# Kernel optimization log

Measured on AMD Instinct MI355X. Metric: run time of the kernel, lower is better.

The kernel has to match this reference:

```python
import jax, jax.numpy as jnp
import numpy as np

EPS_NORM = 1e-12
BN_EPS = 1e-5
TEMP = 0.07


def _l2norm(x, axis):
    n = jnp.sqrt(jnp.sum(x * x, axis=axis, keepdims=True))
    return x / jnp.maximum(n, EPS_NORM)


def _bn_eval(z, w, b):
    # inference-mode BatchNorm2d with running_mean=0, running_var=1
    s = w / jnp.sqrt(jnp.asarray(1.0 + BN_EPS, z.dtype))
    return z * s[None, :, None, None] + b[None, :, None, None]


def setup_inputs() -> dict:
    key = jax.random.key(0)
    ks = jax.random.split(key, 8)
    B, C, H, W = 16, 256, 64, 64
    KD, P = 128, 256
    x = jax.random.normal(ks[0], (B, C, H, W), jnp.float32)
    m_features = jax.random.normal(ks[1], (P, KD), jnp.float32)
    q_w = jax.random.normal(ks[2], (KD, C), jnp.float32) * 0.05
    k_w = jax.random.normal(ks[3], (KD, KD), jnp.float32) * 0.05
    v_w = jax.random.normal(ks[4], (KD, KD), jnp.float32) * 0.05
    o_w = jax.random.normal(ks[5], (C, KD), jnp.float32) * 0.05
    dw_w = jax.random.normal(ks[6], (C, 1, 3, 3), jnp.float32) * 0.1
    return {
        "x": x, "m_features": m_features,
        "q_w": q_w, "q_b": jnp.zeros((KD,), jnp.float32),
        "k_w": k_w, "k_b": jnp.zeros((KD,), jnp.float32),
        "v_w": v_w, "v_b": jnp.zeros((KD,), jnp.float32),
        "o_w": o_w, "o_b": jnp.zeros((C,), jnp.float32),
        "dw_w": dw_w,
        "bn1_w": jnp.ones((C,), jnp.float32), "bn1_b": jnp.zeros((C,), jnp.float32),
        "bn2_w": jnp.ones((C,), jnp.float32), "bn2_b": jnp.zeros((C,), jnp.float32),
        "gamma": jnp.ones((C,), jnp.float32) * 1e-5,
    }


def reference(x, m_features, q_w, q_b, k_w, k_b, v_w, v_b, o_w, o_b,
              dw_w, bn1_w, bn1_b, bn2_w, bn2_b, gamma):
    B, C, H, W = x.shape
    KD = q_w.shape[0]
    residual = x
    # q_proj 1x1 conv -> [B,KD,H,W], L2-normalize over channel dim
    q = jnp.einsum('bchw,kc->bkhw', x, q_w) + q_b[None, :, None, None]
    q = _l2norm(q, axis=1)
    q = q.reshape(B, KD, H * W).transpose(0, 2, 1)  # [B, HW, KD]
    # k/v projections of memory bank [P, KD]
    k = _l2norm(m_features @ k_w.T + k_b, axis=-1)
    v = m_features @ v_w.T + v_b
    # fp32 attention with clamped logits
    q32, k32, v32 = q.astype(jnp.float32), k.astype(jnp.float32), v.astype(jnp.float32)
    logits = jnp.clip(jnp.einsum('bnd,pd->bnp', q32, k32) / TEMP, -30.0, 30.0)
    attn = jax.nn.softmax(logits, axis=-1)
    out = jnp.einsum('bnp,pd->bnd', attn, v32).astype(x.dtype)
    out = out.transpose(0, 2, 1).reshape(B, KD, H, W)
    # out_proj 1x1 conv -> [B,C,H,W]
    out = jnp.einsum('bkhw,ck->bchw', out, o_w) + o_b[None, :, None, None]
    # local branch: depthwise 3x3 conv + BN + exact GELU
    local = jax.lax.conv_general_dilated(
        out, dw_w, window_strides=(1, 1), padding='SAME',
        feature_group_count=C,
        dimension_numbers=('NCHW', 'OIHW', 'NCHW'))
    local = jax.nn.gelu(_bn_eval(local, bn1_w, bn1_b), approximate=False)
    out = out + local
    return _bn_eval(residual + out * gamma[None, :, None, None], bn2_w, bn2_b)
```

## Files before the change

### kernel.cpp

```cpp
#include <hip/hip_runtime.h>
#include <hip/hip_bf16.h>
#include <math.h>

#define B_ 16
#define C_ 256
#define H_ 64
#define W_ 64
#define KD_ 128
#define P_ 256
#define HW_ (H_ * W_)

typedef __bf16 bf16;
typedef float f32x4_t __attribute__((ext_vector_type(4)));
typedef float f32x16_t __attribute__((ext_vector_type(16)));
typedef unsigned char u8;

__device__ __forceinline__ unsigned cvt_pk_fp8_lo(float a, float b, unsigned old) {
#if __has_builtin(__builtin_amdgcn_cvt_pk_fp8_f32)
    return __builtin_amdgcn_cvt_pk_fp8_f32(a, b, old, false);
#else
    unsigned r = old;
    asm("v_cvt_pk_fp8_f32 %0, %1, %2" : "+v"(r) : "v"(a), "v"(b));
    return r;
#endif
}
__device__ __forceinline__ unsigned cvt_pk_fp8_hi(float a, float b, unsigned old) {
#if __has_builtin(__builtin_amdgcn_cvt_pk_fp8_f32)
    return __builtin_amdgcn_cvt_pk_fp8_f32(a, b, old, true);
#else
    unsigned r = old;
    asm("v_cvt_pk_fp8_f32 %0, %1, %2 op_sel:[0,0,1]" : "+v"(r) : "v"(a), "v"(b));
    return r;
#endif
}
__device__ __forceinline__ uint2 pack8_fp8(const float* f) {
    uint2 r;
    r.x = cvt_pk_fp8_hi(f[2], f[3], cvt_pk_fp8_lo(f[0], f[1], 0u));
    r.y = cvt_pk_fp8_hi(f[6], f[7], cvt_pk_fp8_lo(f[4], f[5], 0u));
    return r;
}
template<int SEL>
__device__ __forceinline__ float fp8_to_f32(unsigned w) {
#if __has_builtin(__builtin_amdgcn_cvt_f32_fp8)
    return __builtin_amdgcn_cvt_f32_fp8(w, SEL);
#else
    float r;
    asm("v_cvt_f32_fp8 %0, %1" : "=v"(r) : "v"(w >> (SEL * 8)));
    return r;
#endif
}

__global__ __launch_bounds__(128) void k_prep1(
    const float* __restrict__ m_feat,
    const float* __restrict__ k_w, const float* __restrict__ k_b,
    const float* __restrict__ v_w, const float* __restrict__ v_b,
    float* __restrict__ kn_f, float* __restrict__ v_f)
{
    const int p = blockIdx.x;
    const int j = threadIdx.x;
    __shared__ float msh[KD_];
    __shared__ float red[2];
    msh[j] = m_feat[p * KD_ + j];
    __syncthreads();

    float ka = k_b[j];
    float va = v_b[j];
#pragma unroll 4
    for (int d = 0; d < KD_; ++d) {
        const float m = msh[d];
        ka = fmaf(m, k_w[j * KD_ + d], ka);
        va = fmaf(m, v_w[j * KD_ + d], va);
    }
    float s = ka * ka;
#pragma unroll
    for (int o = 1; o < 64; o <<= 1) s += __shfl_xor(s, o);
    if ((j & 63) == 0) red[j >> 6] = s;
    __syncthreads();
    s = red[0] + red[1];
    const float inv = 1.0f / (0.07f * fmaxf(sqrtf(s), 1e-12f));
    kn_f[p * KD_ + j] = ka * inv;
    v_f[p * KD_ + j] = va;
}

__global__ __launch_bounds__(256) void k_prep23(
    const float* __restrict__ o_w, const float* __restrict__ v_f,
    const float* __restrict__ q_w, const float* __restrict__ kn_f,
    u8* __restrict__ m28, u8* __restrict__ qw8, u8* __restrict__ kn8)
{
    if (blockIdx.x < 256) {
        const int c = blockIdx.x;
        const int p = threadIdx.x;
        __shared__ float osh[KD_];
        if (p < KD_) osh[p] = o_w[c * KD_ + p];
        __syncthreads();
        float acc = 0.f;
#pragma unroll 4
        for (int k = 0; k < KD_; ++k) acc = fmaf(osh[k], v_f[p * KD_ + k], acc);
        const int mt = c >> 5, r = c & 31;
        const int ks = p >> 4, sub = (p >> 3) & 1, jj = p & 7;
        const unsigned pk = cvt_pk_fp8_lo(acc * 16.0f, 0.f, 0u);
        m28[(((mt * 16 + ks) * 64) + sub * 32 + r) * 8 + jj] = (u8)(pk & 0xffu);
    } else {
        const int t = (blockIdx.x - 256) * 256 + threadIdx.x;
        float f[8];
        if (t < 4096) {
            const int lane = t & 63, g = t >> 6, mt = g >> 4, ks = g & 15;
            const int row = mt * 32 + (lane & 31), k0 = ks * 16 + (lane >> 5) * 8;
            const float* src = q_w + row * C_ + k0;
#pragma unroll
            for (int j = 0; j < 8; ++j) f[j] = src[j] * 16.0f;
            ((uint2*)qw8)[t] = pack8_fp8(f);
        } else {
            const int u = t - 4096;
            const int lane = u & 63, g = u >> 6, mt = g >> 3, ks = g & 7;
            const int row = mt * 32 + (lane & 31), k0 = ks * 16 + (lane >> 5) * 8;
            const float* src = kn_f + row * KD_ + k0;
#pragma unroll
            for (int j = 0; j < 8; ++j) f[j] = src[j];
            ((uint2*)kn8)[u] = pack8_fp8(f);
        }
    }
}

__global__ __launch_bounds__(512, 4) void k_attn(
    const float* __restrict__ x,
    const float* __restrict__ q_b, const float* __restrict__ o_b,
    const u8* __restrict__ qw8, const u8* __restrict__ kn8,
    const u8* __restrict__ m28, u8* __restrict__ outf8)
{
    __shared__ __align__(16) char lds[75776];
    char* const xs = lds + 32768;
    float* const ss_lds   = (float*)(lds + 65536);
    float* const pmax_lds = (float*)(lds + 67584);
    float* const sum_lds  = (float*)(lds + 71680);

    const int rp = blockIdx.x;
    const int b = blockIdx.y;
    const int tid = threadIdx.x;
    const int lane = tid & 63;
    const int wid = tid >> 6;
    const int l31 = lane & 31;
    const int kh  = lane >> 5;

    long kna[8];
#pragma unroll
    for (int ks = 0; ks < 8; ++ks)
        kna[ks] = *(const long*)(kn8 + ((wid * 8 + ks) * 64 + lane) * 8);

    {
        const int sub = tid & 31;
        const int ch0 = tid >> 5;
        const float* xb = x + (size_t)b * C_ * HW_ + rp * 128 + sub * 4;
#pragma unroll
        for (int it = 0; it < 16; ++it) {
            const int ch = it * 16 + ch0;
            const f32x4_t v = *(const f32x4_t*)(xb + (size_t)ch * HW_);
            const unsigned w = cvt_pk_fp8_hi(v[2], v[3],
                               cvt_pk_fp8_lo(v[0], v[1], 0u));
            *(unsigned*)(lds + ch * 128 + sub * 4) = w;
        }
    }
    __syncthreads();

    {
        const int p  = tid & 127;
        const int cb = tid >> 7;
#pragma unroll
        for (int g = 0; g < 8; ++g) {
            const int c0 = cb * 64 + g * 8;
            union { u8 by[8]; uint2 u; } pk;
#pragma unroll
            for (int j = 0; j < 8; ++j)
                pk.by[j] = *(const u8*)(lds + (c0 + j) * 128 + p);
            *(uint2*)(xs + p * 256 + (c0 ^ ((p & 31) << 3))) = pk.u;
        }
    }
    __syncthreads();

    const int mtA = wid & 3, nh = wid >> 2;
    {
        f32x16_t qacc0, qacc1;
#pragma unroll
        for (int i = 0; i < 16; ++i) { qacc0[i] = 0.f; qacc1[i] = 0.f; }
#pragma unroll
        for (int ks = 0; ks < 16; ++ks) {
            const long a = *(const long*)(qw8 + ((mtA * 16 + ks) * 64 + lane) * 8);
            const int ko = (ks * 16 + kh * 8) ^ (l31 << 3);
            const long bx0 = *(const long*)(xs + (nh * 64 + l31) * 256 + ko);
            const long bx1 = *(const long*)(xs + (nh * 64 + 32 + l31) * 256 + ko);
            qacc0 = __builtin_amdgcn_mfma_f32_32x32x16_fp8_fp8(a, bx0, qacc0, 0, 0, 0);
            qacc1 = __builtin_amdgcn_mfma_f32_32x32x16_fp8_fp8(a, bx1, qacc1, 0, 0, 0);
        }
#pragma unroll
        for (int nt = 0; nt < 2; ++nt) {
            const int pix = nh * 64 + nt * 32 + l31;
            float ssp = 0.f;
#pragma unroll
            for (int g = 0; g < 4; ++g) {
                const f32x4_t qbv = *(const f32x4_t*)(q_b + mtA * 32 + g * 8 + kh * 4);
#pragma unroll
                for (int i = 0; i < 4; ++i) {
                    float qv = (nt == 0) ? qacc0[g * 4 + i] : qacc1[g * 4 + i];
                    qv += 16.0f * qbv[i];
                    if (nt == 0) qacc0[g * 4 + i] = qv; else qacc1[g * 4 + i] = qv;
                    ssp = fmaf(qv, qv, ssp);
                }
            }
            ssp += __shfl_xor(ssp, 32);
            if (lane < 32) ss_lds[pix * 4 + mtA] = ssp;
#pragma unroll
            for (int g = 0; g < 4; ++g) {
                const float e0 = (nt == 0) ? qacc0[g * 4 + 0] : qacc1[g * 4 + 0];
                const float e1 = (nt == 0) ? qacc0[g * 4 + 1] : qacc1[g * 4 + 1];
                const float e2 = (nt == 0) ? qacc0[g * 4 + 2] : qacc1[g * 4 + 2];
                const float e3 = (nt == 0) ? qacc0[g * 4 + 3] : qacc1[g * 4 + 3];
                const unsigned qw_ = cvt_pk_fp8_hi(e2, e3, cvt_pk_fp8_lo(e0, e1, 0u));
                *(unsigned*)(lds + pix * 128 +
                             ((mtA * 32 + g * 8 + kh * 4) ^ ((l31 & 15) << 3))) = qw_;
            }
        }
    }
    __syncthreads();

    f32x16_t lacc0, lacc1, lacc2, lacc3;
#pragma unroll
    for (int i = 0; i < 16; ++i) { lacc0[i] = 0.f; lacc1[i] = 0.f; lacc2[i] = 0.f; lacc3[i] = 0.f; }
#pragma unroll
    for (int ks = 0; ks < 8; ++ks) {
        const int ko = (ks * 16 + kh * 8) ^ ((l31 & 15) << 3);
        const long bq0 = *(const long*)(lds + (0 * 32 + l31) * 128 + ko);
        const long bq1 = *(const long*)(lds + (1 * 32 + l31) * 128 + ko);
        const long bq2 = *(const long*)(lds + (2 * 32 + l31) * 128 + ko);
        const long bq3 = *(const long*)(lds + (3 * 32 + l31) * 128 + ko);
        lacc0 = __builtin_amdgcn_mfma_f32_32x32x16_fp8_fp8(kna[ks], bq0, lacc0, 0, 0, 0);
        lacc1 = __builtin_amdgcn_mfma_f32_32x32x16_fp8_fp8(kna[ks], bq1, lacc1, 0, 0, 0);
        lacc2 = __builtin_amdgcn_mfma_f32_32x32x16_fp8_fp8(kna[ks], bq2, lacc2, 0, 0, 0);
        lacc3 = __builtin_amdgcn_mfma_f32_32x32x16_fp8_fp8(kna[ks], bq3, lacc3, 0, 0, 0);
    }
#pragma unroll
    for (int nt = 0; nt < 4; ++nt) {
        const int pix = nt * 32 + l31;
        float mx = -1e30f;
#pragma unroll
        for (int i = 0; i < 16; ++i) {
            const float lv = (nt == 0) ? lacc0[i] : (nt == 1) ? lacc1[i]
                           : (nt == 2) ? lacc2[i] : lacc3[i];
            mx = fmaxf(mx, lv);
        }
        mx = fmaxf(mx, __shfl_xor(mx, 32));
        if (lane < 32) pmax_lds[pix * 8 + wid] = mx;
    }
    __syncthreads();

#pragma unroll
    for (int nt = 0; nt < 4; ++nt) {
        const int pix = nt * 32 + l31;
        const f32x4_t s4 = *(const f32x4_t*)(ss_lds + pix * 4);
        const float qinv = 1.0f / fmaxf(sqrtf(s4[0] + s4[1] + s4[2] + s4[3]), 1e-12f);
        const f32x4_t ma = *(const f32x4_t*)(pmax_lds + pix * 8);
        const f32x4_t mb = *(const f32x4_t*)(pmax_lds + pix * 8 + 4);
        const float cof = 5.545177444479562f -
                          fmaxf(fmaxf(fmaxf(ma[0], ma[1]), fmaxf(ma[2], ma[3])),
                                fmaxf(fmaxf(mb[0], mb[1]), fmaxf(mb[2], mb[3]))) * qinv;
        float sm = 0.f;
#pragma unroll
        for (int g = 0; g < 4; ++g) {
            float e[4];
#pragma unroll
            for (int i = 0; i < 4; ++i) {
                const float lv = (nt == 0) ? lacc0[g * 4 + i] : (nt == 1) ? lacc1[g * 4 + i]
                               : (nt == 2) ? lacc2[g * 4 + i] : lacc3[g * 4 + i];
                e[i] = __expf(fmaf(lv, qinv, cof));
                sm += e[i];
            }
            const unsigned ew = cvt_pk_fp8_hi(e[2], e[3],
                                cvt_pk_fp8_lo(e[0], e[1], 0u));
            const int p0 = wid * 32 + g * 8 + kh * 4;
            *(unsigned*)(lds + pix * 256 + (p0 ^ (l31 << 3))) = ew;
        }
        sm += __shfl_xor(sm, 32);
        if (lane < 32) sum_lds[pix * 8 + wid] = sm;
    }
    __syncthreads();

    f32x16_t oacc0, oacc1, oacc2, oacc3;
#pragma unroll
    for (int i = 0; i < 16; ++i) { oacc0[i] = 0.f; oacc1[i] = 0.f; oacc2[i] = 0.f; oacc3[i] = 0.f; }
#pragma unroll
    for (int ks = 0; ks < 16; ++ks) {
        const long a = *(const long*)(m28 + ((wid * 16 + ks) * 64 + lane) * 8);
        const int ko = (ks * 16 + kh * 8);
        const long be0 = *(const long*)(lds + (0 * 32 + l31) * 256 + (ko ^ (l31 << 3)));
        const long be1 = *(const long*)(lds + (1 * 32 + l31) * 256 + (ko ^ (l31 << 3)));
        const long be2 = *(const long*)(lds + (2 * 32 + l31) * 256 + (ko ^ (l31 << 3)));
        const long be3 = *(const long*)(lds + (3 * 32 + l31) * 256 + (ko ^ (l31 << 3)));
        oacc0 = __builtin_amdgcn_mfma_f32_32x32x16_fp8_fp8(a, be0, oacc0, 0, 0, 0);
        oacc1 = __builtin_amdgcn_mfma_f32_32x32x16_fp8_fp8(a, be1, oacc1, 0, 0, 0);
        oacc2 = __builtin_amdgcn_mfma_f32_32x32x16_fp8_fp8(a, be2, oacc2, 0, 0, 0);
        oacc3 = __builtin_amdgcn_mfma_f32_32x32x16_fp8_fp8(a, be3, oacc3, 0, 0, 0);
    }
    {
        u8* const obase = outf8 + (size_t)b * C_ * HW_ + rp * 128;
        f32x4_t obv16[4];
#pragma unroll
        for (int g = 0; g < 4; ++g) {
            const f32x4_t t = *(const f32x4_t*)(o_b + wid * 32 + g * 8 + kh * 4);
            obv16[g] = t * 16.0f;
        }
#pragma unroll
        for (int nt = 0; nt < 4; ++nt) {
            const int p = nt * 32 + l31;
            const f32x4_t sa = *(const f32x4_t*)(sum_lds + p * 8);
            const f32x4_t sb = *(const f32x4_t*)(sum_lds + p * 8 + 4);
            const float rs16 = 1.0f / ((sa[0] + sa[1] + sa[2] + sa[3]) +
                                       (sb[0] + sb[1] + sb[2] + sb[3]));
            u8* const op = obase + p;
#pragma unroll
            for (int g = 0; g < 4; ++g) {
                float o[4];
#pragma unroll
                for (int i = 0; i < 4; ++i) {
                    const float av = (nt == 0) ? oacc0[g * 4 + i] : (nt == 1) ? oacc1[g * 4 + i]
                                   : (nt == 2) ? oacc2[g * 4 + i] : oacc3[g * 4 + i];
                    o[i] = fmaf(av, rs16, obv16[g][i]);
                }
                const unsigned u01 = cvt_pk_fp8_lo(o[0], o[1], 0u);
                const unsigned u23 = cvt_pk_fp8_lo(o[2], o[3], 0u);
                const int c = wid * 32 + g * 8 + kh * 4;
                op[(size_t)(c + 0) * HW_] = (u8)(u01 & 0xff);
                op[(size_t)(c + 1) * HW_] = (u8)((u01 >> 8) & 0xff);
                op[(size_t)(c + 2) * HW_] = (u8)(u23 & 0xff);
                op[(size_t)(c + 3) * HW_] = (u8)((u23 >> 8) & 0xff);
            }
        }
    }
}

__global__ __launch_bounds__(256, 4) void k_post(
    const float* __restrict__ x, const u8* __restrict__ outf8,
    const float* __restrict__ dw_w,
    const float* __restrict__ bn1_w, const float* __restrict__ bn1_b,
    const float* __restrict__ bn2_w, const float* __restrict__ bn2_b,
    const float* __restrict__ gamma, float* __restrict__ y)
{
    __shared__ __align__(16) u8 os8[64 + HW_ + 64];
    u8* const os = os8 + 64;
    const int bc = blockIdx.x;
    const int c = bc & (C_ - 1);
    const int tid = threadIdx.x;

    if (tid < 4)       *(uint4*)&os8[tid * 16] = make_uint4(0, 0, 0, 0);
    else if (tid < 8)  *(uint4*)&os8[64 + HW_ + (tid - 4) * 16] = make_uint4(0, 0, 0, 0);
    *(uint4*)&os[tid * 16] = *(const uint4*)(outf8 + (size_t)bc * HW_ + tid * 16);

    const float cbn = 0.99999500003750f;
    const float s1 = bn1_w[c] * cbn, b1 = bn1_b[c];
    const float s2 = bn2_w[c] * cbn, b2 = bn2_b[c];
    const float g = gamma[c];
    const float gc = g * 0.0625f;
    float kw[9];
#pragma unroll
    for (int j = 0; j < 9; ++j) kw[j] = dw_w[c * 9 + j] * 0.0625f;

    __syncthreads();

    const int q = tid & 15;
    const int c4 = q * 4;
    const int r0 = tid >> 4;
    const float* xc = x + (size_t)bc * HW_;
    float* yc = y + (size_t)bc * HW_;

#pragma unroll
    for (int k = 0; k < 4; ++k) {
        const int r = r0 + k * 16;
        const f32x4_t x4 = *(const f32x4_t*)(xc + r * 64 + c4);
        float vt[6], vm[6], vb[6];
        {
            const int rbt = r * 64, rbm = rbt + 64, rbb = rbt + 128;
            const unsigned uCt = *(const unsigned*)&os8[rbt + c4];
            const unsigned uCm = *(const unsigned*)&os8[rbm + c4];
            const unsigned uCb = *(const unsigned*)&os8[rbb + c4];
            vt[1] = fp8_to_f32<0>(uCt); vt[2] = fp8_to_f32<1>(uCt);
            vt[3] = fp8_to_f32<2>(uCt); vt[4] = fp8_to_f32<3>(uCt);
            vm[1] = fp8_to_f32<0>(uCm); vm[2] = fp8_to_f32<1>(uCm);
            vm[3] = fp8_to_f32<2>(uCm); vm[4] = fp8_to_f32<3>(uCm);
            vb[1] = fp8_to_f32<0>(uCb); vb[2] = fp8_to_f32<1>(uCb);
            vb[3] = fp8_to_f32<2>(uCb); vb[4] = fp8_to_f32<3>(uCb);
            if (q > 0) {
                vt[0] = fp8_to_f32<3>(*(const unsigned*)&os8[rbt + c4 - 4]);
                vm[0] = fp8_to_f32<3>(*(const unsigned*)&os8[rbm + c4 - 4]);
                vb[0] = fp8_to_f32<3>(*(const unsigned*)&os8[rbb + c4 - 4]);
            } else { vt[0] = vm[0] = vb[0] = 0.f; }
            if (q < 15) {
                vt[5] = fp8_to_f32<0>(*(const unsigned*)&os8[rbt + c4 + 4]);
                vm[5] = fp8_to_f32<0>(*(const unsigned*)&os8[rbm + c4 + 4]);
                vb[5] = fp8_to_f32<0>(*(const unsigned*)&os8[rbb + c4 + 4]);
            } else { vt[5] = vm[5] = vb[5] = 0.f; }
        }
        f32x4_t y4;
#pragma unroll
        for (int j = 0; j < 4; ++j) {
            float conv = kw[0] * vt[j];
            conv = fmaf(kw[1], vt[j + 1], conv);
            conv = fmaf(kw[2], vt[j + 2], conv);
            conv = fmaf(kw[3], vm[j], conv);
            conv = fmaf(kw[4], vm[j + 1], conv);
            conv = fmaf(kw[5], vm[j + 2], conv);
            conv = fmaf(kw[6], vb[j], conv);
            conv = fmaf(kw[7], vb[j + 1], conv);
            conv = fmaf(kw[8], vb[j + 2], conv);
            const float t = fmaf(conv, s1, b1);
            const float lg = t / (1.0f + __expf(-1.702f * t));
            y4[j] = fmaf(lg, g, fmaf(vm[j + 1], gc, x4[j])) * s2 + b2;
        }
        *(f32x4_t*)(yc + r * 64 + c4) = y4;
    }
}

extern "C" void kernel_launch(void* const* d_in, const int* in_sizes, int n_in,
                              void* d_out, int out_size, void* d_ws, size_t ws_size,
                              hipStream_t stream)
{
    const float* x     = (const float*)d_in[0];
    const float* m_f   = (const float*)d_in[1];
    const float* q_w   = (const float*)d_in[2];
    const float* q_b   = (const float*)d_in[3];
    const float* k_w   = (const float*)d_in[4];
    const float* k_b   = (const float*)d_in[5];
    const float* v_w   = (const float*)d_in[6];
    const float* v_b   = (const float*)d_in[7];
    const float* o_w   = (const float*)d_in[8];
    const float* o_b   = (const float*)d_in[9];
    const float* dw_w  = (const float*)d_in[10];
    const float* bn1_w = (const float*)d_in[11];
    const float* bn1_b = (const float*)d_in[12];
    const float* bn2_w = (const float*)d_in[13];
    const float* bn2_b = (const float*)d_in[14];
    const float* gamma = (const float*)d_in[15];

    char* ws = (char*)d_ws;
    u8*    qw8   = (u8*)(ws);
    u8*    kn8   = (u8*)(ws + (32 << 10));
    u8*    m28   = (u8*)(ws + (64 << 10));
    u8*    outf8 = (u8*)(ws + (1 << 20));
    float* kn_f  = (float*)(ws + (1 << 20));
    float* v_f   = (float*)(ws + (1 << 20) + (128 << 10));

    k_prep1<<<dim3(P_), dim3(128), 0, stream>>>(m_f, k_w, k_b, v_w, v_b,
                                                kn_f, v_f);
    k_prep23<<<dim3(288), dim3(256), 0, stream>>>(o_w, v_f, q_w, kn_f,
                                                  m28, qw8, kn8);
    k_attn<<<dim3(H_ / 2, B_), dim3(512), 0, stream>>>(x, q_b, o_b, qw8, kn8,
                                                       m28, outf8);
    k_post<<<dim3(B_ * C_), dim3(256), 0, stream>>>(
        x, outf8, dw_w, bn1_w, bn1_b, bn2_w, bn2_b, gamma, (float*)d_out);
}
```

Baseline: 73.99 us.

## Split attention across 16 waves and drop the softmax row-max pass

The attention kernel now runs with 1024 threads, so each wave computes a 32-row by 64-pixel tile instead of holding all K rows for 128 pixels. The x tile is transposed straight into a swizzled pixel-major LDS layout, which removes a staging pass and one barrier. The per-pixel softmax max reduction and its barrier are replaced by a constant offset taken from the analytic upper bound of the normalized logits. This cuts LDS use, barriers and registers per wave, but small exponentials may underflow in FP8 and lose accuracy.

```diff
diff --git a/kernel.cpp b/kernel.cpp
--- a/kernel.cpp
+++ b/kernel.cpp
@@ -122,17 +122,17 @@
     }
 }
 
-__global__ __launch_bounds__(512, 4) void k_attn(
+__global__ __launch_bounds__(1024, 8) void k_attn(
     const float* __restrict__ x,
     const float* __restrict__ q_b, const float* __restrict__ o_b,
     const u8* __restrict__ qw8, const u8* __restrict__ kn8,
     const u8* __restrict__ m28, u8* __restrict__ outf8)
 {
-    __shared__ __align__(16) char lds[75776];
-    char* const xs = lds + 32768;
-    float* const ss_lds   = (float*)(lds + 65536);
-    float* const pmax_lds = (float*)(lds + 67584);
-    float* const sum_lds  = (float*)(lds + 71680);
+    __shared__ __align__(16) char lds[55296];
+    char* const xs   = lds;
+    char* const qbuf = lds + 32768;
+    float* const ss_lds  = (float*)(lds + 49152);
+    float* const sum_lds = (float*)(lds + 51200);
 
     const int rp = blockIdx.x;
     const int b = blockIdx.y;
@@ -141,192 +141,143 @@
     const int wid = tid >> 6;
     const int l31 = lane & 31;
     const int kh  = lane >> 5;
-
-    long kna[8];
-#pragma unroll
-    for (int ks = 0; ks < 8; ++ks)
-        kna[ks] = *(const long*)(kn8 + ((wid * 8 + ks) * 64 + lane) * 8);
+    const int mt = wid >> 1;
+    const int nh = wid & 1;
 
     {
-        const int sub = tid & 31;
-        const int ch0 = tid >> 5;
-        const float* xb = x + (size_t)b * C_ * HW_ + rp * 128 + sub * 4;
-#pragma unroll
-        for (int it = 0; it < 16; ++it) {
-            const int ch = it * 16 + ch0;
+        const int quad = tid & 31;
+        const int chs  = tid >> 5;
+        const float* xb = x + (size_t)b * C_ * HW_ + rp * 128 + quad * 4;
+#pragma unroll
+        for (int it = 0; it < 8; ++it) {
+            const int ch = it * 32 + chs;
             const f32x4_t v = *(const f32x4_t*)(xb + (size_t)ch * HW_);
             const unsigned w = cvt_pk_fp8_hi(v[2], v[3],
                                cvt_pk_fp8_lo(v[0], v[1], 0u));
-            *(unsigned*)(lds + ch * 128 + sub * 4) = w;
+#pragma unroll
+            for (int k = 0; k < 4; ++k) {
+                const int pix = quad * 4 + k;
+                const int swz = ((quad & 7) << 3) | (k << 6);
+                *(u8*)(xs + pix * 256 + (ch ^ swz)) = (u8)(w >> (8 * k));
+            }
         }
     }
     __syncthreads();
 
     {
-        const int p  = tid & 127;
-        const int cb = tid >> 7;
-#pragma unroll
-        for (int g = 0; g < 8; ++g) {
-            const int c0 = cb * 64 + g * 8;
-            union { u8 by[8]; uint2 u; } pk;
-#pragma unroll
-            for (int j = 0; j < 8; ++j)
-                pk.by[j] = *(const u8*)(lds + (c0 + j) * 128 + p);
-            *(uint2*)(xs + p * 256 + (c0 ^ ((p & 31) << 3))) = pk.u;
-        }
-    }
-    __syncthreads();
-
-    const int mtA = wid & 3, nh = wid >> 2;
-    {
-        f32x16_t qacc0, qacc1;
-#pragma unroll
-        for (int i = 0; i < 16; ++i) { qacc0[i] = 0.f; qacc1[i] = 0.f; }
+        const int mtA = wid & 3, nq = wid >> 2;
+        const int pix = nq * 32 + l31;
+        const int swzp = (((pix >> 2) & 7) << 3) | ((pix & 3) << 6);
+        f32x16_t qacc;
+#pragma unroll
+        for (int i = 0; i < 16; ++i) qacc[i] = 0.f;
 #pragma unroll
         for (int ks = 0; ks < 16; ++ks) {
             const long a = *(const long*)(qw8 + ((mtA * 16 + ks) * 64 + lane) * 8);
-            const int ko = (ks * 16 + kh * 8) ^ (l31 << 3);
-            const long bx0 = *(const long*)(xs + (nh * 64 + l31) * 256 + ko);
-            const long bx1 = *(const long*)(xs + (nh * 64 + 32 + l31) * 256 + ko);
-            qacc0 = __builtin_amdgcn_mfma_f32_32x32x16_fp8_fp8(a, bx0, qacc0, 0, 0, 0);
-            qacc1 = __builtin_amdgcn_mfma_f32_32x32x16_fp8_fp8(a, bx1, qacc1, 0, 0, 0);
-        }
-#pragma unroll
-        for (int nt = 0; nt < 2; ++nt) {
-            const int pix = nh * 64 + nt * 32 + l31;
-            float ssp = 0.f;
-#pragma unroll
-            for (int g = 0; g < 4; ++g) {
-                const f32x4_t qbv = *(const f32x4_t*)(q_b + mtA * 32 + g * 8 + kh * 4);
-#pragma unroll
-                for (int i = 0; i < 4; ++i) {
-                    float qv = (nt == 0) ? qacc0[g * 4 + i] : qacc1[g * 4 + i];
-                    qv += 16.0f * qbv[i];
-                    if (nt == 0) qacc0[g * 4 + i] = qv; else qacc1[g * 4 + i] = qv;
-                    ssp = fmaf(qv, qv, ssp);
-                }
+            const long bx = *(const long*)(xs + pix * 256 + ((ks * 16 + kh * 8) ^ swzp));
+            qacc = __builtin_amdgcn_mfma_f32_32x32x16_fp8_fp8(a, bx, qacc, 0, 0, 0);
+        }
+        float ssp = 0.f;
+#pragma unroll
+        for (int g = 0; g < 4; ++g) {
+            const f32x4_t qbv = *(const f32x4_t*)(q_b + mtA * 32 + g * 8 + kh * 4);
+#pragma unroll
+            for (int i = 0; i < 4; ++i) {
+                const float qv = qacc[g * 4 + i] + 16.0f * qbv[i];
+                qacc[g * 4 + i] = qv;
+                ssp = fmaf(qv, qv, ssp);
             }
-            ssp += __shfl_xor(ssp, 32);
-            if (lane < 32) ss_lds[pix * 4 + mtA] = ssp;
-#pragma unroll
-            for (int g = 0; g < 4; ++g) {
-                const float e0 = (nt == 0) ? qacc0[g * 4 + 0] : qacc1[g * 4 + 0];
-                const float e1 = (nt == 0) ? qacc0[g * 4 + 1] : qacc1[g * 4 + 1];
-                const float e2 = (nt == 0) ? qacc0[g * 4 + 2] : qacc1[g * 4 + 2];
-                const float e3 = (nt == 0) ? qacc0[g * 4 + 3] : qacc1[g * 4 + 3];
-                const unsigned qw_ = cvt_pk_fp8_hi(e2, e3, cvt_pk_fp8_lo(e0, e1, 0u));
-                *(unsigned*)(lds + pix * 128 +
-                             ((mtA * 32 + g * 8 + kh * 4) ^ ((l31 & 15) << 3))) = qw_;
-            }
-        }
-    }
-    __syncthreads();
-
-    f32x16_t lacc0, lacc1, lacc2, lacc3;
-#pragma unroll
-    for (int i = 0; i < 16; ++i) { lacc0[i] = 0.f; lacc1[i] = 0.f; lacc2[i] = 0.f; lacc3[i] = 0.f; }
+        }
+        ssp += __shfl_xor(ssp, 32);
+        if (lane < 32) ss_lds[pix * 4 + mtA] = ssp;
+#pragma unroll
+        for (int g = 0; g < 4; ++g) {
+            const unsigned qw_ = cvt_pk_fp8_hi(qacc[g * 4 + 2], qacc[g * 4 + 3],
+                                 cvt_pk_fp8_lo(qacc[g * 4 + 0], qacc[g * 4 + 1], 0u));
+            *(unsigned*)(qbuf + pix * 128 +
+                         ((mtA * 32 + g * 8 + kh * 4) ^ ((l31 & 15) << 3))) = qw_;
+        }
+    }
+    __syncthreads();
+
+    f32x16_t lacc0, lacc1;
+#pragma unroll
+    for (int i = 0; i < 16; ++i) { lacc0[i] = 0.f; lacc1[i] = 0.f; }
 #pragma unroll
     for (int ks = 0; ks < 8; ++ks) {
+        const long a = *(const long*)(kn8 + ((mt * 8 + ks) * 64 + lane) * 8);
         const int ko = (ks * 16 + kh * 8) ^ ((l31 & 15) << 3);
-        const long bq0 = *(const long*)(lds + (0 * 32 + l31) * 128 + ko);
-        const long bq1 = *(const long*)(lds + (1 * 32 + l31) * 128 + ko);
-        const long bq2 = *(const long*)(lds + (2 * 32 + l31) * 128 + ko);
-        const long bq3 = *(const long*)(lds + (3 * 32 + l31) * 128 + ko);
-        lacc0 = __builtin_amdgcn_mfma_f32_32x32x16_fp8_fp8(kna[ks], bq0, lacc0, 0, 0, 0);
-        lacc1 = __builtin_amdgcn_mfma_f32_32x32x16_fp8_fp8(kna[ks], bq1, lacc1, 0, 0, 0);
-        lacc2 = __builtin_amdgcn_mfma_f32_32x32x16_fp8_fp8(kna[ks], bq2, lacc2, 0, 0, 0);
-        lacc3 = __builtin_amdgcn_mfma_f32_32x32x16_fp8_fp8(kna[ks], bq3, lacc3, 0, 0, 0);
-    }
-#pragma unroll
-    for (int nt = 0; nt < 4; ++nt) {
-        const int pix = nt * 32 + l31;
-        float mx = -1e30f;
-#pragma unroll
-        for (int i = 0; i < 16; ++i) {
-            const float lv = (nt == 0) ? lacc0[i] : (nt == 1) ? lacc1[i]
-                           : (nt == 2) ? lacc2[i] : lacc3[i];
-            mx = fmaxf(mx, lv);
-        }
-        mx = fmaxf(mx, __shfl_xor(mx, 32));
-        if (lane < 32) pmax_lds[pix * 8 + wid] = mx;
-    }
-    __syncthreads();
-
-#pragma unroll
-    for (int nt = 0; nt < 4; ++nt) {
-        const int pix = nt * 32 + l31;
+        const long bq0 = *(const long*)(qbuf + (nh * 64 + 0 * 32 + l31) * 128 + ko);
+        const long bq1 = *(const long*)(qbuf + (nh * 64 + 1 * 32 + l31) * 128 + ko);
+        lacc0 = __builtin_amdgcn_mfma_f32_32x32x16_fp8_fp8(a, bq0, lacc0, 0, 0, 0);
+        lacc1 = __builtin_amdgcn_mfma_f32_32x32x16_fp8_fp8(a, bq1, lacc1, 0, 0, 0);
+    }
+
+#pragma unroll
+    for (int nt = 0; nt < 2; ++nt) {
+        const int pix = nh * 64 + nt * 32 + l31;
         const f32x4_t s4 = *(const f32x4_t*)(ss_lds + pix * 4);
         const float qinv = 1.0f / fmaxf(sqrtf(s4[0] + s4[1] + s4[2] + s4[3]), 1e-12f);
-        const f32x4_t ma = *(const f32x4_t*)(pmax_lds + pix * 8);
-        const f32x4_t mb = *(const f32x4_t*)(pmax_lds + pix * 8 + 4);
-        const float cof = 5.545177444479562f -
-                          fmaxf(fmaxf(fmaxf(ma[0], ma[1]), fmaxf(ma[2], ma[3])),
-                                fmaxf(fmaxf(mb[0], mb[1]), fmaxf(mb[2], mb[3]))) * qinv;
+        const float cof = -8.740536912452074f;
         float sm = 0.f;
 #pragma unroll
         for (int g = 0; g < 4; ++g) {
             float e[4];
 #pragma unroll
             for (int i = 0; i < 4; ++i) {
-                const float lv = (nt == 0) ? lacc0[g * 4 + i] : (nt == 1) ? lacc1[g * 4 + i]
-                               : (nt == 2) ? lacc2[g * 4 + i] : lacc3[g * 4 + i];
+                const float lv = (nt == 0) ? lacc0[g * 4 + i] : lacc1[g * 4 + i];
                 e[i] = __expf(fmaf(lv, qinv, cof));
                 sm += e[i];
             }
             const unsigned ew = cvt_pk_fp8_hi(e[2], e[3],
                                 cvt_pk_fp8_lo(e[0], e[1], 0u));
-            const int p0 = wid * 32 + g * 8 + kh * 4;
-            *(unsigned*)(lds + pix * 256 + (p0 ^ (l31 << 3))) = ew;
+            const int p0 = mt * 32 + g * 8 + kh * 4;
+            *(unsigned*)(xs + pix * 256 + (p0 ^ (l31 << 3))) = ew;
         }
         sm += __shfl_xor(sm, 32);
-        if (lane < 32) sum_lds[pix * 8 + wid] = sm;
-    }
-    __syncthreads();
-
-    f32x16_t oacc0, oacc1, oacc2, oacc3;
-#pragma unroll
-    for (int i = 0; i < 16; ++i) { oacc0[i] = 0.f; oacc1[i] = 0.f; oacc2[i] = 0.f; oacc3[i] = 0.f; }
+        if (lane < 32) sum_lds[pix * 8 + mt] = sm;
+    }
+    __syncthreads();
+
+    f32x16_t oacc0, oacc1;
+#pragma unroll
+    for (int i = 0; i < 16; ++i) { oacc0[i] = 0.f; oacc1[i] = 0.f; }
 #pragma unroll
     for (int ks = 0; ks < 16; ++ks) {
-        const long a = *(const long*)(m28 + ((wid * 16 + ks) * 64 + lane) * 8);
-        const int ko = (ks * 16 + kh * 8);
-        const long be0 = *(const long*)(lds + (0 * 32 + l31) * 256 + (ko ^ (l31 << 3)));
-        const long be1 = *(const long*)(lds + (1 * 32 + l31) * 256 + (ko ^ (l31 << 3)));
-        const long be2 = *(const long*)(lds + (2 * 32 + l31) * 256 + (ko ^ (l31 << 3)));
-        const long be3 = *(const long*)(lds + (3 * 32 + l31) * 256 + (ko ^ (l31 << 3)));
+        const long a = *(const long*)(m28 + ((mt * 16 + ks) * 64 + lane) * 8);
+        const int ko = ks * 16 + kh * 8;
+        const long be0 = *(const long*)(xs + (nh * 64 + 0 * 32 + l31) * 256 + (ko ^ (l31 << 3)));
+        const long be1 = *(const long*)(xs + (nh * 64 + 1 * 32 + l31) * 256 + (ko ^ (l31 << 3)));
         oacc0 = __builtin_amdgcn_mfma_f32_32x32x16_fp8_fp8(a, be0, oacc0, 0, 0, 0);
         oacc1 = __builtin_amdgcn_mfma_f32_32x32x16_fp8_fp8(a, be1, oacc1, 0, 0, 0);
-        oacc2 = __builtin_amdgcn_mfma_f32_32x32x16_fp8_fp8(a, be2, oacc2, 0, 0, 0);
-        oacc3 = __builtin_amdgcn_mfma_f32_32x32x16_fp8_fp8(a, be3, oacc3, 0, 0, 0);
     }
     {
         u8* const obase = outf8 + (size_t)b * C_ * HW_ + rp * 128;
         f32x4_t obv16[4];
 #pragma unroll
         for (int g = 0; g < 4; ++g) {
-            const f32x4_t t = *(const f32x4_t*)(o_b + wid * 32 + g * 8 + kh * 4);
+            const f32x4_t t = *(const f32x4_t*)(o_b + mt * 32 + g * 8 + kh * 4);
             obv16[g] = t * 16.0f;
         }
 #pragma unroll
-        for (int nt = 0; nt < 4; ++nt) {
-            const int p = nt * 32 + l31;
+        for (int nt = 0; nt < 2; ++nt) {
+            const int p = nh * 64 + nt * 32 + l31;
             const f32x4_t sa = *(const f32x4_t*)(sum_lds + p * 8);
             const f32x4_t sb = *(const f32x4_t*)(sum_lds + p * 8 + 4);
-            const float rs16 = 1.0f / ((sa[0] + sa[1] + sa[2] + sa[3]) +
-                                       (sb[0] + sb[1] + sb[2] + sb[3]));
+            const float rs = 1.0f / ((sa[0] + sa[1] + sa[2] + sa[3]) +
+                                     (sb[0] + sb[1] + sb[2] + sb[3]));
             u8* const op = obase + p;
 #pragma unroll
             for (int g = 0; g < 4; ++g) {
                 float o[4];
 #pragma unroll
                 for (int i = 0; i < 4; ++i) {
-                    const float av = (nt == 0) ? oacc0[g * 4 + i] : (nt == 1) ? oacc1[g * 4 + i]
-                                   : (nt == 2) ? oacc2[g * 4 + i] : oacc3[g * 4 + i];
-                    o[i] = fmaf(av, rs16, obv16[g][i]);
+                    const float av = (nt == 0) ? oacc0[g * 4 + i] : oacc1[g * 4 + i];
+                    o[i] = fmaf(av, rs, obv16[g][i]);
                 }
                 const unsigned u01 = cvt_pk_fp8_lo(o[0], o[1], 0u);
                 const unsigned u23 = cvt_pk_fp8_lo(o[2], o[3], 0u);
-                const int c = wid * 32 + g * 8 + kh * 4;
+                const int c = mt * 32 + g * 8 + kh * 4;
                 op[(size_t)(c + 0) * HW_] = (u8)(u01 & 0xff);
                 op[(size_t)(c + 1) * HW_] = (u8)((u01 >> 8) & 0xff);
                 op[(size_t)(c + 2) * HW_] = (u8)(u23 & 0xff);
@@ -443,15 +394,15 @@
     u8*    kn8   = (u8*)(ws + (32 << 10));
     u8*    m28   = (u8*)(ws + (64 << 10));
     u8*    outf8 = (u8*)(ws + (1 << 20));
-    float* kn_f  = (float*)(ws + (1 << 20));
-    float* v_f   = (float*)(ws + (1 << 20) + (128 << 10));
+    float* kn_f  = (float*)(ws + (18 << 20));
+    float* v_f   = (float*)(ws + (18 << 20) + (128 << 10));
 
     k_prep1<<<dim3(P_), dim3(128), 0, stream>>>(m_f, k_w, k_b, v_w, v_b,
                                                 kn_f, v_f);
     k_prep23<<<dim3(288), dim3(256), 0, stream>>>(o_w, v_f, q_w, kn_f,
                                                   m28, qw8, kn8);
-    k_attn<<<dim3(H_ / 2, B_), dim3(512), 0, stream>>>(x, q_b, o_b, qw8, kn8,
-                                                       m28, outf8);
+    k_attn<<<dim3(H_ / 2, B_), dim3(1024), 0, stream>>>(x, q_b, o_b, qw8, kn8,
+                                                        m28, outf8);
     k_post<<<dim3(B_ * C_), dim3(256), 0, stream>>>(
         x, outf8, dw_w, bn1_w, bn1_b, bn2_w, bn2_b, gamma, (float*)d_out);
 }
```

After: 83.25 us. 12.5% more time.

## Double attention tile to 256 pixels per block with 1024 threads

Applied to the files above, without the earlier changes.

The attention kernel now handles 256 pixels per workgroup with 16 waves instead of 128 pixels with 8 waves. Each key/value m-tile is shared by two waves, each covering one pixel half. The grid is halved to 16x16 blocks and LDS usage roughly doubles to about 148 KB. Workspace offsets for kn_f/v_f move so they no longer alias outf8. The aim is fewer blocks and better amortization of the per-block weight loads, at the cost of occupancy: the large LDS footprint allows about one block per CU and leaves only 256 blocks for the device.

```diff
diff --git a/kernel.cpp b/kernel.cpp
--- a/kernel.cpp
+++ b/kernel.cpp
@@ -122,62 +122,62 @@
     }
 }
 
-__global__ __launch_bounds__(512, 4) void k_attn(
+__global__ __launch_bounds__(1024, 4) void k_attn(
     const float* __restrict__ x,
     const float* __restrict__ q_b, const float* __restrict__ o_b,
     const u8* __restrict__ qw8, const u8* __restrict__ kn8,
     const u8* __restrict__ m28, u8* __restrict__ outf8)
 {
-    __shared__ __align__(16) char lds[75776];
-    char* const xs = lds + 32768;
-    float* const ss_lds   = (float*)(lds + 65536);
-    float* const pmax_lds = (float*)(lds + 67584);
-    float* const sum_lds  = (float*)(lds + 71680);
-
-    const int rp = blockIdx.x;
+    __shared__ __align__(16) char lds[151552];
+    char* const xs = lds + 65536;
+    float* const ss_lds   = (float*)(lds + 131072);
+    float* const pmax_lds = (float*)(lds + 135168);
+    float* const sum_lds  = (float*)(lds + 143360);
+
+    const int rq = blockIdx.x;
     const int b = blockIdx.y;
     const int tid = threadIdx.x;
     const int lane = tid & 63;
     const int wid = tid >> 6;
     const int l31 = lane & 31;
     const int kh  = lane >> 5;
+    const int mt = wid >> 1;
+    const int half = wid & 1;
 
     long kna[8];
 #pragma unroll
     for (int ks = 0; ks < 8; ++ks)
-        kna[ks] = *(const long*)(kn8 + ((wid * 8 + ks) * 64 + lane) * 8);
+        kna[ks] = *(const long*)(kn8 + ((mt * 8 + ks) * 64 + lane) * 8);
 
     {
-        const int sub = tid & 31;
-        const int ch0 = tid >> 5;
-        const float* xb = x + (size_t)b * C_ * HW_ + rp * 128 + sub * 4;
+        const float* xb = x + (size_t)b * C_ * HW_ + rq * 256 + lane * 4;
 #pragma unroll
         for (int it = 0; it < 16; ++it) {
-            const int ch = it * 16 + ch0;
+            const int ch = it * 16 + wid;
             const f32x4_t v = *(const f32x4_t*)(xb + (size_t)ch * HW_);
             const unsigned w = cvt_pk_fp8_hi(v[2], v[3],
                                cvt_pk_fp8_lo(v[0], v[1], 0u));
-            *(unsigned*)(lds + ch * 128 + sub * 4) = w;
+            *(unsigned*)(lds + ch * 256 + lane * 4) = w;
         }
     }
     __syncthreads();
 
     {
-        const int p  = tid & 127;
-        const int cb = tid >> 7;
+        const int p  = tid & 255;
+        const int cb = tid >> 8;
 #pragma unroll
         for (int g = 0; g < 8; ++g) {
             const int c0 = cb * 64 + g * 8;
             union { u8 by[8]; uint2 u; } pk;
 #pragma unroll
             for (int j = 0; j < 8; ++j)
-                pk.by[j] = *(const u8*)(lds + (c0 + j) * 128 + p);
+                pk.by[j] = *(const u8*)(lds + (c0 + j) * 256 + p);
             *(uint2*)(xs + p * 256 + (c0 ^ ((p & 31) << 3))) = pk.u;
         }
     }
     __syncthreads();
 
-    const int mtA = wid & 3, nh = wid >> 2;
+    const int mtA = wid & 3, np = wid >> 2;
     {
         f32x16_t qacc0, qacc1;
 #pragma unroll
@@ -186,14 +186,14 @@
         for (int ks = 0; ks < 16; ++ks) {
             const long a = *(const long*)(qw8 + ((mtA * 16 + ks) * 64 + lane) * 8);
             const int ko = (ks * 16 + kh * 8) ^ (l31 << 3);
-            const long bx0 = *(const long*)(xs + (nh * 64 + l31) * 256 + ko);
-            const long bx1 = *(const long*)(xs + (nh * 64 + 32 + l31) * 256 + ko);
+            const long bx0 = *(const long*)(xs + (np * 64 + l31) * 256 + ko);
+            const long bx1 = *(const long*)(xs + (np * 64 + 32 + l31) * 256 + ko);
             qacc0 = __builtin_amdgcn_mfma_f32_32x32x16_fp8_fp8(a, bx0, qacc0, 0, 0, 0);
             qacc1 = __builtin_amdgcn_mfma_f32_32x32x16_fp8_fp8(a, bx1, qacc1, 0, 0, 0);
         }
 #pragma unroll
         for (int nt = 0; nt < 2; ++nt) {
-            const int pix = nh * 64 + nt * 32 + l31;
+            const int pix = np * 64 + nt * 32 + l31;
             float ssp = 0.f;
 #pragma unroll
             for (int g = 0; g < 4; ++g) {
@@ -228,10 +228,10 @@
 #pragma unroll
     for (int ks = 0; ks < 8; ++ks) {
         const int ko = (ks * 16 + kh * 8) ^ ((l31 & 15) << 3);
-        const long bq0 = *(const long*)(lds + (0 * 32 + l31) * 128 + ko);
-        const long bq1 = *(const long*)(lds + (1 * 32 + l31) * 128 + ko);
-        const long bq2 = *(const long*)(lds + (2 * 32 + l31) * 128 + ko);
-        const long bq3 = *(const long*)(lds + (3 * 32 + l31) * 128 + ko);
+        const long bq0 = *(const long*)(lds + (half * 128 + 0 * 32 + l31) * 128 + ko);
+        const long bq1 = *(const long*)(lds + (half * 128 + 1 * 32 + l31) * 128 + ko);
+        const long bq2 = *(const long*)(lds + (half * 128 + 2 * 32 + l31) * 128 + ko);
+        const long bq3 = *(const long*)(lds + (half * 128 + 3 * 32 + l31) * 128 + ko);
         lacc0 = __builtin_amdgcn_mfma_f32_32x32x16_fp8_fp8(kna[ks], bq0, lacc0, 0, 0, 0);
         lacc1 = __builtin_amdgcn_mfma_f32_32x32x16_fp8_fp8(kna[ks], bq1, lacc1, 0, 0, 0);
         lacc2 = __builtin_amdgcn_mfma_f32_32x32x16_fp8_fp8(kna[ks], bq2, lacc2, 0, 0, 0);
@@ -239,7 +239,7 @@
     }
 #pragma unroll
     for (int nt = 0; nt < 4; ++nt) {
-        const int pix = nt * 32 + l31;
+        const int pix = half * 128 + nt * 32 + l31;
         float mx = -1e30f;
 #pragma unroll
         for (int i = 0; i < 16; ++i) {
@@ -248,13 +248,13 @@
             mx = fmaxf(mx, lv);
         }
         mx = fmaxf(mx, __shfl_xor(mx, 32));
-        if (lane < 32) pmax_lds[pix * 8 + wid] = mx;
+        if (lane < 32) pmax_lds[pix * 8 + mt] = mx;
     }
     __syncthreads();
 
 #pragma unroll
     for (int nt = 0; nt < 4; ++nt) {
-        const int pix = nt * 32 + l31;
+        const int pix = half * 128 + nt * 32 + l31;
         const f32x4_t s4 = *(const f32x4_t*)(ss_lds + pix * 4);
         const float qinv = 1.0f / fmaxf(sqrtf(s4[0] + s4[1] + s4[2] + s4[3]), 1e-12f);
         const f32x4_t ma = *(const f32x4_t*)(pmax_lds + pix * 8);
@@ -275,11 +275,11 @@
             }
             const unsigned ew = cvt_pk_fp8_hi(e[2], e[3],
                                 cvt_pk_fp8_lo(e[0], e[1], 0u));
-            const int p0 = wid * 32 + g * 8 + kh * 4;
+            const int p0 = mt * 32 + g * 8 + kh * 4;
             *(unsigned*)(lds + pix * 256 + (p0 ^ (l31 << 3))) = ew;
         }
         sm += __shfl_xor(sm, 32);
-        if (lane < 32) sum_lds[pix * 8 + wid] = sm;
+        if (lane < 32) sum_lds[pix * 8 + mt] = sm;
     }
     __syncthreads();
 
@@ -288,32 +288,32 @@
     for (int i = 0; i < 16; ++i) { oacc0[i] = 0.f; oacc1[i] = 0.f; oacc2[i] = 0.f; oacc3[i] = 0.f; }
 #pragma unroll
     for (int ks = 0; ks < 16; ++ks) {
-        const long a = *(const long*)(m28 + ((wid * 16 + ks) * 64 + lane) * 8);
-        const int ko = (ks * 16 + kh * 8);
-        const long be0 = *(const long*)(lds + (0 * 32 + l31) * 256 + (ko ^ (l31 << 3)));
-        const long be1 = *(const long*)(lds + (1 * 32 + l31) * 256 + (ko ^ (l31 << 3)));
-        const long be2 = *(const long*)(lds + (2 * 32 + l31) * 256 + (ko ^ (l31 << 3)));
-        const long be3 = *(const long*)(lds + (3 * 32 + l31) * 256 + (ko ^ (l31 << 3)));
+        const long a = *(const long*)(m28 + ((mt * 16 + ks) * 64 + lane) * 8);
+        const int ko = ks * 16 + kh * 8;
+        const long be0 = *(const long*)(lds + (half * 128 + 0 * 32 + l31) * 256 + (ko ^ (l31 << 3)));
+        const long be1 = *(const long*)(lds + (half * 128 + 1 * 32 + l31) * 256 + (ko ^ (l31 << 3)));
+        const long be2 = *(const long*)(lds + (half * 128 + 2 * 32 + l31) * 256 + (ko ^ (l31 << 3)));
+        const long be3 = *(const long*)(lds + (half * 128 + 3 * 32 + l31) * 256 + (ko ^ (l31 << 3)));
         oacc0 = __builtin_amdgcn_mfma_f32_32x32x16_fp8_fp8(a, be0, oacc0, 0, 0, 0);
         oacc1 = __builtin_amdgcn_mfma_f32_32x32x16_fp8_fp8(a, be1, oacc1, 0, 0, 0);
         oacc2 = __builtin_amdgcn_mfma_f32_32x32x16_fp8_fp8(a, be2, oacc2, 0, 0, 0);
         oacc3 = __builtin_amdgcn_mfma_f32_32x32x16_fp8_fp8(a, be3, oacc3, 0, 0, 0);
     }
     {
-        u8* const obase = outf8 + (size_t)b * C_ * HW_ + rp * 128;
+        u8* const obase = outf8 + (size_t)b * C_ * HW_ + rq * 256;
         f32x4_t obv16[4];
 #pragma unroll
         for (int g = 0; g < 4; ++g) {
-            const f32x4_t t = *(const f32x4_t*)(o_b + wid * 32 + g * 8 + kh * 4);
+            const f32x4_t t = *(const f32x4_t*)(o_b + mt * 32 + g * 8 + kh * 4);
             obv16[g] = t * 16.0f;
         }
 #pragma unroll
         for (int nt = 0; nt < 4; ++nt) {
-            const int p = nt * 32 + l31;
+            const int p = half * 128 + nt * 32 + l31;
             const f32x4_t sa = *(const f32x4_t*)(sum_lds + p * 8);
             const f32x4_t sb = *(const f32x4_t*)(sum_lds + p * 8 + 4);
-            const float rs16 = 1.0f / ((sa[0] + sa[1] + sa[2] + sa[3]) +
-                                       (sb[0] + sb[1] + sb[2] + sb[3]));
+            const float rs = 1.0f / ((sa[0] + sa[1] + sa[2] + sa[3]) +
+                                     (sb[0] + sb[1] + sb[2] + sb[3]));
             u8* const op = obase + p;
 #pragma unroll
             for (int g = 0; g < 4; ++g) {
@@ -322,11 +322,11 @@
                 for (int i = 0; i < 4; ++i) {
                     const float av = (nt == 0) ? oacc0[g * 4 + i] : (nt == 1) ? oacc1[g * 4 + i]
                                    : (nt == 2) ? oacc2[g * 4 + i] : oacc3[g * 4 + i];
-                    o[i] = fmaf(av, rs16, obv16[g][i]);
+                    o[i] = fmaf(av, rs, obv16[g][i]);
                 }
                 const unsigned u01 = cvt_pk_fp8_lo(o[0], o[1], 0u);
                 const unsigned u23 = cvt_pk_fp8_lo(o[2], o[3], 0u);
-                const int c = wid * 32 + g * 8 + kh * 4;
+                const int c = mt * 32 + g * 8 + kh * 4;
                 op[(size_t)(c + 0) * HW_] = (u8)(u01 & 0xff);
                 op[(size_t)(c + 1) * HW_] = (u8)((u01 >> 8) & 0xff);
                 op[(size_t)(c + 2) * HW_] = (u8)(u23 & 0xff);
@@ -443,15 +443,15 @@
     u8*    kn8   = (u8*)(ws + (32 << 10));
     u8*    m28   = (u8*)(ws + (64 << 10));
     u8*    outf8 = (u8*)(ws + (1 << 20));
-    float* kn_f  = (float*)(ws + (1 << 20));
-    float* v_f   = (float*)(ws + (1 << 20) + (128 << 10));
+    float* kn_f  = (float*)(ws + (18 << 20));
+    float* v_f   = (float*)(ws + (18 << 20) + (128 << 10));
 
     k_prep1<<<dim3(P_), dim3(128), 0, stream>>>(m_f, k_w, k_b, v_w, v_b,
                                                 kn_f, v_f);
     k_prep23<<<dim3(288), dim3(256), 0, stream>>>(o_w, v_f, q_w, kn_f,
                                                   m28, qw8, kn8);
-    k_attn<<<dim3(H_ / 2, B_), dim3(512), 0, stream>>>(x, q_b, o_b, qw8, kn8,
-                                                       m28, outf8);
+    k_attn<<<dim3(16, B_), dim3(1024), 0, stream>>>(x, q_b, o_b, qw8, kn8,
+                                                    m28, outf8);
     k_post<<<dim3(B_ * C_), dim3(256), 0, stream>>>(
         x, outf8, dw_w, bn1_w, bn1_b, bn2_w, bn2_b, gamma, (float*)d_out);
 }
```

New measurement: 78.90 us. 6.6% more time.
